# Kernel optimization log

Measured on AMD Instinct MI355X. Metric: run time of the kernel, lower is better.

The kernel has to match this reference:

```python
import jax, jax.numpy as jnp
import numpy as np

T = 2048          # tokens (flattened prefill)
H = 3584          # hidden_size
NH = 16           # num query heads
NKV = 8           # num kv heads
G = NH // NKV     # GQA group size
D = 256           # head_dim
SCALE = 256.0 ** -0.5   # query_pre_attn_scalar ** -0.5
WINDOW = 1024     # sliding_window_size
CAP = 50.0        # logit softcap
BASE = 10000.0    # rope theta
NEG = -1e30


def _rope(x, positions):
    # x: [T, n, D], neox-style rotary over full head_dim
    half = D // 2
    inv_freq = 1.0 / (BASE ** (jnp.arange(0, D, 2, dtype=jnp.float32) / D))  # [half]
    ang = positions.astype(jnp.float32)[:, None] * inv_freq  # [T, half]
    cos = jnp.cos(ang)[:, None, :]  # [T,1,half]
    sin = jnp.sin(ang)[:, None, :]
    x1, x2 = x[..., :half], x[..., half:]
    return jnp.concatenate([x1 * cos - x2 * sin, x2 * cos + x1 * sin], axis=-1)


def setup_inputs() -> dict:
    key = jax.random.key(0)
    ks = jax.random.split(key, 5)
    s = 0.02
    return {
        "hidden_states": jax.random.normal(ks[0], (T, H), dtype=jnp.float32),
        "Wq": jax.random.normal(ks[1], (H, NH * D), dtype=jnp.float32) * s,
        "Wk": jax.random.normal(ks[2], (H, NKV * D), dtype=jnp.float32) * s,
        "Wv": jax.random.normal(ks[3], (H, NKV * D), dtype=jnp.float32) * s,
        "Wo": jax.random.normal(ks[4], (NH * D, H), dtype=jnp.float32) * s,
        "positions": jnp.arange(T, dtype=jnp.int32),
    }


def reference(hidden_states, Wq, Wk, Wv, Wo, positions):
    q = (hidden_states @ Wq).reshape(T, NH, D)
    k = (hidden_states @ Wk).reshape(T, NKV, D)
    v = (hidden_states @ Wv).reshape(T, NKV, D)
    q = _rope(q, positions)
    k = _rope(k, positions)

    # GQA attention: group query heads over kv heads
    qg = (q * SCALE).reshape(T, NKV, G, D)
    scores = jnp.einsum('qhgd,khd->hgqk', qg, k)  # [NKV,G,T,T]
    scores = CAP * jnp.tanh(scores / CAP)         # logit softcap

    i = jnp.arange(T)[:, None]
    j = jnp.arange(T)[None, :]
    mask = (j <= i) & (i - j < WINDOW)            # causal + sliding window
    scores = jnp.where(mask, scores, NEG)

    p = jax.nn.softmax(scores, axis=-1)
    o = jnp.einsum('hgqk,khd->qhgd', p, v).reshape(T, NH * D)
    return o @ Wo
```

## Files before the change

### kernel.cpp

```cpp
#include <hip/hip_runtime.h>
#include <math.h>

typedef __attribute__((ext_vector_type(8))) __bf16 bf16x8;
typedef __attribute__((ext_vector_type(4))) __bf16 bf16x4;
typedef __attribute__((ext_vector_type(4))) float f32x4;

#define TSEQ 2048
#define HDIM 3584
#define NQH  16
#define NKVH 8
#define DH   256
#define WIN  1024
#define QKD  (NQH * DH)
#define KVD  (NKVH * DH)
#define QKVN 8192

#define MFMA __builtin_amdgcn_mfma_f32_16x16x32_bf16

__device__ __forceinline__ void gload_lds16(const void* g, void* l) {
  __builtin_amdgcn_global_load_lds(
      (const __attribute__((address_space(1))) void*)g,
      (__attribute__((address_space(3))) void*)l, 16, 0, 0);
}


__global__ void cvt_bf16_kernel(const float* __restrict__ in,
                                __bf16* __restrict__ out, long n) {
  long i = ((long)blockIdx.x * blockDim.x + threadIdx.x) * 4;
  if (i >= n) return;
  float4 v = *reinterpret_cast<const float4*>(in + i);
  bf16x4 o4;
  o4.x = (__bf16)v.x; o4.y = (__bf16)v.y; o4.z = (__bf16)v.z; o4.w = (__bf16)v.w;
  *reinterpret_cast<bf16x4*>(out + i) = o4;
}

__global__ void transpose_all_kernel(const float* __restrict__ Wq,
                                     const float* __restrict__ Wk,
                                     const float* __restrict__ Wv,
                                     const float* __restrict__ Wo,
                                     __bf16* __restrict__ WqT,
                                     __bf16* __restrict__ WkT,
                                     __bf16* __restrict__ WvT,
                                     __bf16* __restrict__ WoT) {
  __shared__ float tile[64][65];
  int id = blockIdx.x;
  const float* src; __bf16* dst; int R, C;
  if (id < 3584)      { src = Wq; dst = WqT; R = HDIM; C = QKD; }
  else if (id < 5376) { id -= 3584; src = Wk; dst = WkT; R = HDIM; C = KVD; }
  else if (id < 7168) { id -= 5376; src = Wv; dst = WvT; R = HDIM; C = KVD; }
  else                { id -= 7168; src = Wo; dst = WoT; R = QKD; C = HDIM; }
  const int nbx = C >> 6;
  const int c0 = (id % nbx) * 64, r0 = (id / nbx) * 64;
  const int tid = threadIdx.x;
#pragma unroll
  for (int it = 0; it < 4; ++it) {
    int f = tid + it * 256;
    int row = f >> 4, c4 = (f & 15) * 4;
    float4 v = *reinterpret_cast<const float4*>(&src[(size_t)(r0 + row) * C + c0 + c4]);
    tile[row][c4] = v.x; tile[row][c4 + 1] = v.y;
    tile[row][c4 + 2] = v.z; tile[row][c4 + 3] = v.w;
  }
  __syncthreads();
#pragma unroll
  for (int it = 0; it < 2; ++it) {
    int s = tid + it * 256;
    int oc = s >> 3, rb = (s & 7) * 8;
    bf16x8 o8;
#pragma unroll
    for (int j = 0; j < 8; ++j) o8[j] = (__bf16)tile[rb + j][oc];
    *reinterpret_cast<bf16x8*>(&dst[(size_t)(c0 + oc) * R + r0 + rb]) = o8;
  }
}

__global__ void transpose_bf16_kernel(const __bf16* __restrict__ in,
                                      __bf16* __restrict__ out, int ldin, int ldout) {
  __shared__ __bf16 tile[32][33];
  const int tx = threadIdx.x, ty = threadIdx.y;
  const int c0 = blockIdx.x * 32, r0 = blockIdx.y * 32;
#pragma unroll
  for (int i = 0; i < 4; ++i)
    tile[ty + i * 8][tx] = in[(size_t)(r0 + ty + i * 8) * ldin + (c0 + tx)];
  __syncthreads();
#pragma unroll
  for (int i = 0; i < 4; ++i)
    out[(size_t)(c0 + ty + i * 8) * ldout + (r0 + tx)] = tile[tx][ty + i * 8];
}

__global__ void rope_table_kernel(const int* __restrict__ positions,
                                  float* __restrict__ ct,
                                  float* __restrict__ st) {
  int i = blockIdx.x * blockDim.x + threadIdx.x;
  if (i >= TSEQ * 128) return;
  int t = i >> 7, j = i & 127;
  float invf = (float)exp((double)(-2 * j) * (9.210340371976184 / 256.0));
  float ang = (float)positions[t] * invf;
  ct[i] = cosf(ang);
  st[i] = sinf(ang);
}

__global__ void rope_qk_kernel(__bf16* __restrict__ qkv,
                               const float* __restrict__ ct,
                               const float* __restrict__ st) {
  int i = blockIdx.x * blockDim.x + threadIdx.x;
  int j = i & 127;
  int th = i >> 7;
  int t = th / 24;
  int hh = th - t * 24;
  float scale = (hh < 16) ? 0.0625f : 1.0f;
  size_t base = (size_t)t * QKVN + ((hh < 16) ? hh * DH : QKD + (hh - 16) * DH) + j;
  float x1 = (float)qkv[base], x2 = (float)qkv[base + 128];
  float c = ct[(t << 7) + j], s = st[(t << 7) + j];
  qkv[base]       = (__bf16)((x1 * c - x2 * s) * scale);
  qkv[base + 128] = (__bf16)((x2 * c + x1 * s) * scale);
}

__global__ void reduce2_kernel(const __bf16* __restrict__ p0,
                               const __bf16* __restrict__ p1,
                               float* __restrict__ out, int n8) {
  int stride = gridDim.x * blockDim.x;
  for (int i = blockIdx.x * blockDim.x + threadIdx.x; i < n8; i += stride) {
    bf16x8 a = reinterpret_cast<const bf16x8*>(p0)[i];
    bf16x8 b = reinterpret_cast<const bf16x8*>(p1)[i];
    float4 o0, o1;
    o0.x = (float)a[0] + (float)b[0]; o0.y = (float)a[1] + (float)b[1];
    o0.z = (float)a[2] + (float)b[2]; o0.w = (float)a[3] + (float)b[3];
    o1.x = (float)a[4] + (float)b[4]; o1.y = (float)a[5] + (float)b[5];
    o1.z = (float)a[6] + (float)b[6]; o1.w = (float)a[7] + (float)b[7];
    reinterpret_cast<float4*>(out)[2 * i] = o0;
    reinterpret_cast<float4*>(out)[2 * i + 1] = o1;
  }
}


__device__ __forceinline__ void stage_half(const __bf16* __restrict__ gbase,
                                           int row0, int ldg, int k0,
                                           __bf16* lds_half, int tid) {
  const int lane = tid & 63;
  const int w = tid >> 6;
  const int lr = lane >> 3;
  const int swzcol = ((lane & 7) ^ lr) << 3;
  const __bf16* g = gbase + (size_t)(row0 + w * 8 + lr) * ldg + k0 + swzcol;
  __bf16* l = lds_half + w * 512;
  gload_lds16(g, l);
  gload_lds16(g + (size_t)64 * ldg, l + 4096);
}

#define BAR __builtin_amdgcn_s_barrier()

#define RD_A(DST, BASE, MO)                                         \
  _Pragma("unroll")                                                 \
  for (int m_ = 0; m_ < 4; ++m_) {                                  \
    const __bf16* p_ = (BASE) + (((MO) + m_) * 16 + l15) * 64;      \
    DST[m_][0] = *(const bf16x8*)(p_ + kxa);                        \
    DST[m_][1] = *(const bf16x8*)(p_ + kxb);                        \
  }

#define RD_B(DST, BASE, NO)                                         \
  _Pragma("unroll")                                                 \
  for (int n_ = 0; n_ < 2; ++n_) {                                  \
    const __bf16* p_ = (BASE) + (bro + ((NO) + n_) * 16 + l15) * 64;\
    DST[n_][0] = *(const bf16x8*)(p_ + kxa);                        \
    DST[n_][1] = *(const bf16x8*)(p_ + kxb);                        \
  }

#define MQUAD(AF, BF, MO, NO)                                          \
  __builtin_amdgcn_s_setprio(1);                                       \
  _Pragma("unroll")                                                    \
  for (int m_ = 0; m_ < 4; ++m_)                                       \
    _Pragma("unroll")                                                  \
    for (int n_ = 0; n_ < 2; ++n_) {                                   \
      acc[(MO) + m_][(NO) + n_] =                                      \
          MFMA(AF[m_][0], BF[n_][0], acc[(MO) + m_][(NO) + n_], 0, 0, 0); \
      acc[(MO) + m_][(NO) + n_] =                                      \
          MFMA(AF[m_][1], BF[n_][1], acc[(MO) + m_][(NO) + n_], 0, 0, 0); \
    }                                                                  \
  __builtin_amdgcn_s_setprio(0);

template <typename CT>
__global__ __launch_bounds__(512, 2) void gemm256_kernel(
    const __bf16* __restrict__ A, const __bf16* __restrict__ B,
    CT* __restrict__ C, int lda, int Klen, int ldc, int nrc, size_t cstride) {
  __shared__ __bf16 lds[2][2][2][8192];

  const int nwg = gridDim.x;
  const int per = nwg >> 3;
  const int wg = (blockIdx.x & 7) * per + (blockIdx.x >> 3);
  const int kslice = wg / nrc;
  const int rem = wg - kslice * nrc;
  const int row0 = (rem & 7) * 256;
  const int col0 = (rem >> 3) * 256;
  const int k0 = kslice * Klen;
  CT* Cs = C + (size_t)kslice * cstride;

  const int tid = threadIdx.x;
  const int lane = tid & 63, w = tid >> 6;
  const int wr = w >> 2, wc = w & 3;
  const int l15 = lane & 15, lg = lane >> 4;
  const int swz = (lane & 7) << 3;
  const int kxa = (lg * 8) ^ swz;
  const int kxb = (32 + lg * 8) ^ swz;
  const int bro = (wc & 1) * 64;

  const __bf16* Ablk = A + (size_t)row0 * lda + k0;
  const __bf16* Bblk = B + (size_t)col0 * lda + k0;

  const __bf16* Ae = &lds[0][0][wr][0];
  const __bf16* Be = &lds[0][1][wc >> 1][0];
  const __bf16* Ao = &lds[1][0][wr][0];
  const __bf16* Bo = &lds[1][1][wc >> 1][0];

  f32x4 acc[8][4] = {};
  const int NT = Klen >> 6;
  const int NI = NT >> 1;

  stage_half(Ablk, 0,   lda, 0,  &lds[0][0][0][0], tid);
  stage_half(Ablk, 128, lda, 0,  &lds[0][0][1][0], tid);
  stage_half(Bblk, 0,   lda, 0,  &lds[0][1][0][0], tid);
  stage_half(Bblk, 128, lda, 0,  &lds[0][1][1][0], tid);
  stage_half(Ablk, 0,   lda, 64, &lds[1][0][0][0], tid);
  stage_half(Ablk, 128, lda, 64, &lds[1][0][1][0], tid);
  asm volatile("s_waitcnt vmcnt(4)" ::: "memory");
  BAR;

  bf16x8 a03[4][2], a47[4][2], b01[2][2], b23[2][2];

  for (int j = 0; j < NI; ++j) {
    const int e = 2 * j, o = 2 * j + 1;
    const bool last = (j == NI - 1);

    RD_A(a03, Ae, 0);
    RD_B(b01, Be, 0);
    stage_half(Bblk, 0, lda, o * 64, &lds[1][1][0][0], tid);
    asm volatile("s_waitcnt lgkmcnt(8)" ::: "memory");
    BAR; MQUAD(a03, b01, 0, 0); BAR;

    RD_A(a47, Ae, 4);
    stage_half(Bblk, 128, lda, o * 64, &lds[1][1][1][0], tid);
    BAR; MQUAD(a47, b01, 4, 0); BAR;

    RD_B(b23, Be, 2);
    if (!last) stage_half(Ablk, 0, lda, (e + 2) * 64, &lds[0][0][0][0], tid);
    BAR; MQUAD(a47, b23, 4, 2); BAR;

    if (!last) {
      stage_half(Ablk, 128, lda, (e + 2) * 64, &lds[0][0][1][0], tid);
      asm volatile("s_waitcnt vmcnt(4)" ::: "memory");
    } else {
      asm volatile("s_waitcnt vmcnt(0)" ::: "memory");
    }
    BAR; MQUAD(a03, b23, 0, 2); BAR;

    RD_A(a03, Ao, 0);
    RD_B(b01, Bo, 0);
    if (!last) stage_half(Bblk, 0, lda, (e + 2) * 64, &lds[0][1][0][0], tid);
    asm volatile("s_waitcnt lgkmcnt(8)" ::: "memory");
    BAR; MQUAD(a03, b01, 0, 0); BAR;

    RD_A(a47, Ao, 4);
    if (!last) stage_half(Bblk, 128, lda, (e + 2) * 64, &lds[0][1][1][0], tid);
    BAR; MQUAD(a47, b01, 4, 0); BAR;

    RD_B(b23, Bo, 2);
    if (!last) stage_half(Ablk, 0, lda, (o + 2) * 64, &lds[1][0][0][0], tid);
    BAR; MQUAD(a47, b23, 4, 2); BAR;

    if (!last) {
      stage_half(Ablk, 128, lda, (o + 2) * 64, &lds[1][0][1][0], tid);
      asm volatile("s_waitcnt vmcnt(4)" ::: "memory");
    }
    BAR; MQUAD(a03, b23, 0, 2); BAR;
  }

#pragma unroll
  for (int m = 0; m < 8; ++m)
#pragma unroll
    for (int n = 0; n < 4; ++n)
#pragma unroll
      for (int r = 0; r < 4; ++r) {
        int row = row0 + wr * 128 + m * 16 + lg * 4 + r;
        int col = col0 + wc * 64 + n * 16 + l15;
        Cs[(size_t)row * ldc + col] = (CT)acc[m][n][r];
      }
}


__device__ __forceinline__ void attn_stage(const __bf16* __restrict__ kg,
                                           const __bf16* __restrict__ vg,
                                           __bf16* Kd, __bf16* Vd, int tid) {
  const int ktr = tid >> 5;
  const int kslot = (tid & 31) ^ ktr;
  const __bf16* ks = kg + (size_t)ktr * QKVN + kslot * 8;
  __bf16* kd = Kd + tid * 8;
  const int vtr = (tid >> 3) & 7;
  const int vslot = (tid & 7) ^ vtr;
  const __bf16* vs = vg + (size_t)(tid >> 3) * TSEQ + vslot * 8;
  __bf16* vd = Vd + tid * 8;
#pragma unroll
  for (int i = 0; i < 8; ++i) {
    gload_lds16(ks + (size_t)(i * 8) * QKVN, kd + i * 2048);
    gload_lds16(vs + (size_t)(i * 32) * TSEQ, vd + i * 2048);
  }
}

__global__ __launch_bounds__(256, 1) void attn_kernel(
    const __bf16* __restrict__ q, const __bf16* __restrict__ k,
    const __bf16* __restrict__ vt, __bf16* __restrict__ o) {
  __shared__ __bf16 Klds[2][64][256];
  __shared__ __bf16 Vlds[2][256][64];
  __shared__ __bf16 Plds[4][2][16][72];

  const int tid = threadIdx.x;
  const int wave = tid >> 6;
  const int lane = tid & 63;
  const int l16 = lane & 15;
  const int lg = lane >> 4;
  const int h = blockIdx.x;
  const int qh = 2 * h + (wave >> 1);
  const int q0 = blockIdx.y << 6;
  const int qr = q0 + (wave & 1) * 32;

  const __bf16* kg0 = k + (size_t)h * DH;
  const __bf16* vg0 = vt + (size_t)(h * DH) * TSEQ;

  int t_lo = q0 - (WIN - 1);
  if (t_lo < 0) t_lo = 0;
  t_lo &= ~63;
  const int NTile = ((q0 - t_lo) >> 6) + 1;

  attn_stage(kg0 + (size_t)t_lo * QKVN, vg0 + t_lo, &Klds[0][0][0], &Vlds[0][0][0], tid);

  bf16x8 qf[2][8];
#pragma unroll
  for (int g = 0; g < 2; ++g) {
    const __bf16* qp = q + (size_t)(qr + 16 * g + l16) * QKVN + qh * DH + lg * 8;
#pragma unroll
    for (int ds = 0; ds < 8; ++ds)
      qf[g][ds] = *reinterpret_cast<const bf16x8*>(qp + ds * 32);
  }

  f32x4 accO[2][16] = {};
  float l_run[2][4] = {};

  for (int it = 0; it < NTile; ++it) {
    const int t0 = t_lo + it * 64;
    const int cur = it & 1;

    if (it + 1 < NTile) {
      attn_stage(kg0 + (size_t)(t0 + 64) * QKVN, vg0 + (t0 + 64),
                 &Klds[cur ^ 1][0][0], &Vlds[cur ^ 1][0][0], tid);
      asm volatile("s_waitcnt vmcnt(16)" ::: "memory");
    } else {
      asm volatile("s_waitcnt vmcnt(0)" ::: "memory");
    }
    __builtin_amdgcn_s_barrier();

    const __bf16* Kc = &Klds[cur][0][0];
    const __bf16* Vc = &Vlds[cur][0][0];

    f32x4 accS[2][4] = {};
#pragma unroll
    for (int ds = 0; ds < 8; ++ds)
#pragma unroll
      for (int nt = 0; nt < 4; ++nt) {
        int row = nt * 16 + l16;
        int slot = (4 * ds + lg) ^ (l16 & 7);
        bf16x8 kf = *reinterpret_cast<const bf16x8*>(Kc + row * 256 + slot * 8);
        accS[0][nt] = MFMA(qf[0][ds], kf, accS[0][nt], 0, 0, 0);
        accS[1][nt] = MFMA(qf[1][ds], kf, accS[1][nt], 0, 0, 0);
      }

#pragma unroll
    for (int g = 0; g < 2; ++g) {
      float rs[4] = {0.f, 0.f, 0.f, 0.f};
#pragma unroll
      for (int nt = 0; nt < 4; ++nt) {
        int key = t0 + nt * 16 + l16;
#pragma unroll
        for (int r = 0; r < 4; ++r) {
          int row = qr + 16 * g + lg * 4 + r;
          float t = __expf(accS[g][nt][r] * 0.04f);
          float p = __expf(-100.0f / (t + 1.0f));
          bool valid = (key <= row) && (row - key < WIN);
          p = valid ? p : 0.f;
          rs[r] += p;
          Plds[wave][g][lg * 4 + r][nt * 16 + l16] = (__bf16)p;
        }
      }
#pragma unroll
      for (int off = 1; off < 16; off <<= 1)
#pragma unroll
        for (int r = 0; r < 4; ++r)
          rs[r] += __shfl_xor(rs[r], off);
#pragma unroll
      for (int r = 0; r < 4; ++r)
        l_run[g][r] += rs[r];
    }

#pragma unroll
    for (int ks = 0; ks < 2; ++ks) {
      bf16x8 pa0 = *reinterpret_cast<const bf16x8*>(&Plds[wave][0][l16][ks * 32 + lg * 8]);
      bf16x8 pa1 = *reinterpret_cast<const bf16x8*>(&Plds[wave][1][l16][ks * 32 + lg * 8]);
#pragma unroll
      for (int nt2 = 0; nt2 < 16; ++nt2) {
        int row = nt2 * 16 + l16;
        int slot = (4 * ks + lg) ^ (l16 & 7);
        bf16x8 vb = *reinterpret_cast<const bf16x8*>(Vc + row * 64 + slot * 8);
        accO[0][nt2] = MFMA(pa0, vb, accO[0][nt2], 0, 0, 0);
        accO[1][nt2] = MFMA(pa1, vb, accO[1][nt2], 0, 0, 0);
      }
    }
    __builtin_amdgcn_s_barrier();
  }

#pragma unroll
  for (int g = 0; g < 2; ++g)
#pragma unroll
    for (int r = 0; r < 4; ++r) {
      float inv_l = 1.f / l_run[g][r];
      int row = qr + 16 * g + lg * 4 + r;
#pragma unroll
      for (int nt2 = 0; nt2 < 16; ++nt2)
        o[(size_t)row * QKD + qh * DH + nt2 * 16 + l16] = (__bf16)(accO[g][nt2][r] * inv_l);
    }
}


extern "C" void kernel_launch(void* const* d_in, const int* in_sizes, int n_in,
                              void* d_out, int out_size, void* d_ws, size_t ws_size,
                              hipStream_t stream) {
  const float* hs = (const float*)d_in[0];
  const float* Wq = (const float*)d_in[1];
  const float* Wk = (const float*)d_in[2];
  const float* Wv = (const float*)d_in[3];
  const float* Wo = (const float*)d_in[4];
  const int* positions = (const int*)d_in[5];
  float* out = (float*)d_out;

  char* ws = (char*)d_ws;
  const size_t SZ_HS  = (size_t)TSEQ * HDIM * 2;
  const size_t SZ_WQT = (size_t)QKD * HDIM * 2;
  const size_t SZ_WKT = (size_t)KVD * HDIM * 2;
  const size_t SZ_WOT = (size_t)HDIM * QKD * 2;
  const size_t SZ_QKV = (size_t)TSEQ * QKVN * 2;
  const size_t SZ_O   = (size_t)TSEQ * QKD * 2;
  const size_t SZ_TBL = (size_t)TSEQ * 128 * 4;

  __bf16* hs_bf = (__bf16*)ws; ws += SZ_HS;
  __bf16* WqT   = (__bf16*)ws; ws += SZ_WQT;
  __bf16* WkT   = (__bf16*)ws; ws += SZ_WKT;
  __bf16* WvT   = (__bf16*)ws; ws += SZ_WKT;
  __bf16* WoT   = (__bf16*)ws; ws += SZ_WOT;
  __bf16* qkv   = (__bf16*)ws; ws += SZ_QKV;
  __bf16* o_bf  = (__bf16*)ws; ws += SZ_O;
  float*  cost  = (float*)ws;  ws += SZ_TBL;
  float*  sint  = (float*)ws;  ws += SZ_TBL;
  __bf16* vt_bf = hs_bf;
  __bf16* cpart = WqT;
  if ((size_t)(ws - (char*)d_ws) > ws_size) return;

  cvt_bf16_kernel<<<(TSEQ * HDIM) / 1024, 256, 0, stream>>>(hs, hs_bf, (long)TSEQ * HDIM);
  transpose_all_kernel<<<10752, 256, 0, stream>>>(Wq, Wk, Wv, Wo, WqT, WkT, WvT, WoT);
  rope_table_kernel<<<(TSEQ * 128) / 256, 256, 0, stream>>>(positions, cost, sint);

  gemm256_kernel<__bf16><<<256, 512, 0, stream>>>(hs_bf, WqT, qkv, HDIM, HDIM, QKVN, 256, 0);

  rope_qk_kernel<<<(TSEQ * 24 * 128) / 256, 256, 0, stream>>>(qkv, cost, sint);
  transpose_bf16_kernel<<<dim3(KVD / 32, TSEQ / 32), dim3(32, 8), 0, stream>>>(qkv + QKD + KVD, vt_bf, QKVN, TSEQ);

  attn_kernel<<<dim3(NKVH, TSEQ / 64), 256, 0, stream>>>(qkv, qkv + QKD, vt_bf, o_bf);

  gemm256_kernel<__bf16><<<224, 512, 0, stream>>>(o_bf, WoT, cpart, QKD, QKD / 2, HDIM, 112,
                                                  (size_t)TSEQ * HDIM);
  reduce2_kernel<<<2048, 256, 0, stream>>>(cpart, cpart + (size_t)TSEQ * HDIM, out,
                                           TSEQ * HDIM / 8);
}
```

Measured before the change: 340.4 us.

## Double attention waves per block and vectorize RoPE kernel

The attention kernel now runs 8 waves per block, each owning 16 query rows instead of 32. This halves per-wave accumulator registers and adds more waves to hide latency, and the K/V staging is split across 512 threads. MFMA phases are wrapped in s_setprio raises. The RoPE kernel now processes 8 elements per thread with 128-bit loads and stores. The cost is that each K/V fragment in LDS is read by twice as many waves, raising LDS traffic per MFMA.

```diff
diff --git a/kernel.cpp b/kernel.cpp
--- a/kernel.cpp
+++ b/kernel.cpp
@@ -102,16 +102,26 @@
                                const float* __restrict__ ct,
                                const float* __restrict__ st) {
   int i = blockIdx.x * blockDim.x + threadIdx.x;
-  int j = i & 127;
-  int th = i >> 7;
+  int jg = (i & 15) * 8;
+  int th = i >> 4;
   int t = th / 24;
   int hh = th - t * 24;
   float scale = (hh < 16) ? 0.0625f : 1.0f;
-  size_t base = (size_t)t * QKVN + ((hh < 16) ? hh * DH : QKD + (hh - 16) * DH) + j;
-  float x1 = (float)qkv[base], x2 = (float)qkv[base + 128];
-  float c = ct[(t << 7) + j], s = st[(t << 7) + j];
-  qkv[base]       = (__bf16)((x1 * c - x2 * s) * scale);
-  qkv[base + 128] = (__bf16)((x2 * c + x1 * s) * scale);
+  size_t base = (size_t)t * QKVN + ((hh < 16) ? hh * DH : QKD + (hh - 16) * DH) + jg;
+  bf16x8 x1 = *reinterpret_cast<const bf16x8*>(qkv + base);
+  bf16x8 x2 = *reinterpret_cast<const bf16x8*>(qkv + base + 128);
+  const float* cp = ct + (t << 7) + jg;
+  const float* sp = st + (t << 7) + jg;
+  bf16x8 o1, o2;
+#pragma unroll
+  for (int e = 0; e < 8; ++e) {
+    float c = cp[e], s = sp[e];
+    float a = (float)x1[e], b = (float)x2[e];
+    o1[e] = (__bf16)((a * c - b * s) * scale);
+    o2[e] = (__bf16)((b * c + a * s) * scale);
+  }
+  *reinterpret_cast<bf16x8*>(qkv + base) = o1;
+  *reinterpret_cast<bf16x8*>(qkv + base + 128) = o2;
 }
 
 __global__ void reduce2_kernel(const __bf16* __restrict__ p0,
@@ -287,27 +297,22 @@
 __device__ __forceinline__ void attn_stage(const __bf16* __restrict__ kg,
                                            const __bf16* __restrict__ vg,
                                            __bf16* Kd, __bf16* Vd, int tid) {
-  const int ktr = tid >> 5;
-  const int kslot = (tid & 31) ^ ktr;
-  const __bf16* ks = kg + (size_t)ktr * QKVN + kslot * 8;
-  __bf16* kd = Kd + tid * 8;
-  const int vtr = (tid >> 3) & 7;
-  const int vslot = (tid & 7) ^ vtr;
-  const __bf16* vs = vg + (size_t)(tid >> 3) * TSEQ + vslot * 8;
-  __bf16* vd = Vd + tid * 8;
-#pragma unroll
-  for (int i = 0; i < 8; ++i) {
-    gload_lds16(ks + (size_t)(i * 8) * QKVN, kd + i * 2048);
-    gload_lds16(vs + (size_t)(i * 32) * TSEQ, vd + i * 2048);
-  }
-}
-
-__global__ __launch_bounds__(256, 1) void attn_kernel(
+#pragma unroll
+  for (int i = 0; i < 4; ++i) {
+    int c = tid + i * 512;
+    int krow = c >> 5, kslot = c & 31;
+    gload_lds16(kg + (size_t)krow * QKVN + ((kslot ^ (krow & 7)) * 8), Kd + c * 8);
+    int vrow = c >> 3, vslot = c & 7;
+    gload_lds16(vg + (size_t)vrow * TSEQ + ((vslot ^ (vrow & 7)) * 8), Vd + c * 8);
+  }
+}
+
+__global__ __launch_bounds__(512, 1) void attn_kernel(
     const __bf16* __restrict__ q, const __bf16* __restrict__ k,
     const __bf16* __restrict__ vt, __bf16* __restrict__ o) {
   __shared__ __bf16 Klds[2][64][256];
   __shared__ __bf16 Vlds[2][256][64];
-  __shared__ __bf16 Plds[4][2][16][72];
+  __shared__ __bf16 Plds[8][16][72];
 
   const int tid = threadIdx.x;
   const int wave = tid >> 6;
@@ -315,9 +320,9 @@
   const int l16 = lane & 15;
   const int lg = lane >> 4;
   const int h = blockIdx.x;
-  const int qh = 2 * h + (wave >> 1);
+  const int qh = 2 * h + (wave >> 2);
   const int q0 = blockIdx.y << 6;
-  const int qr = q0 + (wave & 1) * 32;
+  const int qr = q0 + (wave & 3) * 16;
 
   const __bf16* kg0 = k + (size_t)h * DH;
   const __bf16* vg0 = vt + (size_t)(h * DH) * TSEQ;
@@ -329,17 +334,16 @@
 
   attn_stage(kg0 + (size_t)t_lo * QKVN, vg0 + t_lo, &Klds[0][0][0], &Vlds[0][0][0], tid);
 
-  bf16x8 qf[2][8];
-#pragma unroll
-  for (int g = 0; g < 2; ++g) {
-    const __bf16* qp = q + (size_t)(qr + 16 * g + l16) * QKVN + qh * DH + lg * 8;
+  bf16x8 qf[8];
+  {
+    const __bf16* qp = q + (size_t)(qr + l16) * QKVN + qh * DH + lg * 8;
 #pragma unroll
     for (int ds = 0; ds < 8; ++ds)
-      qf[g][ds] = *reinterpret_cast<const bf16x8*>(qp + ds * 32);
-  }
-
-  f32x4 accO[2][16] = {};
-  float l_run[2][4] = {};
+      qf[ds] = *reinterpret_cast<const bf16x8*>(qp + ds * 32);
+  }
+
+  f32x4 accO[16] = {};
+  float l_run[4] = {0.f, 0.f, 0.f, 0.f};
 
   for (int it = 0; it < NTile; ++it) {
     const int t0 = t_lo + it * 64;
@@ -348,7 +352,7 @@
     if (it + 1 < NTile) {
       attn_stage(kg0 + (size_t)(t0 + 64) * QKVN, vg0 + (t0 + 64),
                  &Klds[cur ^ 1][0][0], &Vlds[cur ^ 1][0][0], tid);
-      asm volatile("s_waitcnt vmcnt(16)" ::: "memory");
+      asm volatile("s_waitcnt vmcnt(8)" ::: "memory");
     } else {
       asm volatile("s_waitcnt vmcnt(0)" ::: "memory");
     }
@@ -357,7 +361,8 @@
     const __bf16* Kc = &Klds[cur][0][0];
     const __bf16* Vc = &Vlds[cur][0][0];
 
-    f32x4 accS[2][4] = {};
+    f32x4 accS[4] = {};
+    __builtin_amdgcn_s_setprio(1);
 #pragma unroll
     for (int ds = 0; ds < 8; ++ds)
 #pragma unroll
@@ -365,63 +370,58 @@
         int row = nt * 16 + l16;
         int slot = (4 * ds + lg) ^ (l16 & 7);
         bf16x8 kf = *reinterpret_cast<const bf16x8*>(Kc + row * 256 + slot * 8);
-        accS[0][nt] = MFMA(qf[0][ds], kf, accS[0][nt], 0, 0, 0);
-        accS[1][nt] = MFMA(qf[1][ds], kf, accS[1][nt], 0, 0, 0);
+        accS[nt] = MFMA(qf[ds], kf, accS[nt], 0, 0, 0);
       }
-
-#pragma unroll
-    for (int g = 0; g < 2; ++g) {
-      float rs[4] = {0.f, 0.f, 0.f, 0.f};
-#pragma unroll
-      for (int nt = 0; nt < 4; ++nt) {
-        int key = t0 + nt * 16 + l16;
-#pragma unroll
-        for (int r = 0; r < 4; ++r) {
-          int row = qr + 16 * g + lg * 4 + r;
-          float t = __expf(accS[g][nt][r] * 0.04f);
-          float p = __expf(-100.0f / (t + 1.0f));
-          bool valid = (key <= row) && (row - key < WIN);
-          p = valid ? p : 0.f;
-          rs[r] += p;
-          Plds[wave][g][lg * 4 + r][nt * 16 + l16] = (__bf16)p;
-        }
+    __builtin_amdgcn_s_setprio(0);
+
+    float rs[4] = {0.f, 0.f, 0.f, 0.f};
+#pragma unroll
+    for (int nt = 0; nt < 4; ++nt) {
+      int key = t0 + nt * 16 + l16;
+#pragma unroll
+      for (int r = 0; r < 4; ++r) {
+        int row = qr + lg * 4 + r;
+        float t = __expf(accS[nt][r] * 0.04f);
+        float p = __expf(-100.0f / (t + 1.0f));
+        bool valid = (key <= row) && (row - key < WIN);
+        p = valid ? p : 0.f;
+        rs[r] += p;
+        Plds[wave][lg * 4 + r][nt * 16 + l16] = (__bf16)p;
       }
-#pragma unroll
-      for (int off = 1; off < 16; off <<= 1)
-#pragma unroll
-        for (int r = 0; r < 4; ++r)
-          rs[r] += __shfl_xor(rs[r], off);
+    }
+#pragma unroll
+    for (int off = 1; off < 16; off <<= 1)
 #pragma unroll
       for (int r = 0; r < 4; ++r)
-        l_run[g][r] += rs[r];
-    }
-
+        rs[r] += __shfl_xor(rs[r], off);
+#pragma unroll
+    for (int r = 0; r < 4; ++r)
+      l_run[r] += rs[r];
+
+    __builtin_amdgcn_s_setprio(1);
 #pragma unroll
     for (int ks = 0; ks < 2; ++ks) {
-      bf16x8 pa0 = *reinterpret_cast<const bf16x8*>(&Plds[wave][0][l16][ks * 32 + lg * 8]);
-      bf16x8 pa1 = *reinterpret_cast<const bf16x8*>(&Plds[wave][1][l16][ks * 32 + lg * 8]);
+      bf16x8 pa = *reinterpret_cast<const bf16x8*>(&Plds[wave][l16][ks * 32 + lg * 8]);
 #pragma unroll
       for (int nt2 = 0; nt2 < 16; ++nt2) {
         int row = nt2 * 16 + l16;
         int slot = (4 * ks + lg) ^ (l16 & 7);
         bf16x8 vb = *reinterpret_cast<const bf16x8*>(Vc + row * 64 + slot * 8);
-        accO[0][nt2] = MFMA(pa0, vb, accO[0][nt2], 0, 0, 0);
-        accO[1][nt2] = MFMA(pa1, vb, accO[1][nt2], 0, 0, 0);
+        accO[nt2] = MFMA(pa, vb, accO[nt2], 0, 0, 0);
       }
     }
+    __builtin_amdgcn_s_setprio(0);
     __builtin_amdgcn_s_barrier();
   }
 
 #pragma unroll
-  for (int g = 0; g < 2; ++g)
-#pragma unroll
-    for (int r = 0; r < 4; ++r) {
-      float inv_l = 1.f / l_run[g][r];
-      int row = qr + 16 * g + lg * 4 + r;
-#pragma unroll
-      for (int nt2 = 0; nt2 < 16; ++nt2)
-        o[(size_t)row * QKD + qh * DH + nt2 * 16 + l16] = (__bf16)(accO[g][nt2][r] * inv_l);
-    }
+  for (int r = 0; r < 4; ++r) {
+    float inv_l = 1.f / l_run[r];
+    int row = qr + lg * 4 + r;
+#pragma unroll
+    for (int nt2 = 0; nt2 < 16; ++nt2)
+      o[(size_t)row * QKD + qh * DH + nt2 * 16 + l16] = (__bf16)(accO[nt2][r] * inv_l);
+  }
 }
 
 
@@ -464,10 +464,10 @@
 
   gemm256_kernel<__bf16><<<256, 512, 0, stream>>>(hs_bf, WqT, qkv, HDIM, HDIM, QKVN, 256, 0);
 
-  rope_qk_kernel<<<(TSEQ * 24 * 128) / 256, 256, 0, stream>>>(qkv, cost, sint);
+  rope_qk_kernel<<<(TSEQ * 24 * 16) / 256, 256, 0, stream>>>(qkv, cost, sint);
   transpose_bf16_kernel<<<dim3(KVD / 32, TSEQ / 32), dim3(32, 8), 0, stream>>>(qkv + QKD + KVD, vt_bf, QKVN, TSEQ);
 
-  attn_kernel<<<dim3(NKVH, TSEQ / 64), 256, 0, stream>>>(qkv, qkv + QKD, vt_bf, o_bf);
+  attn_kernel<<<dim3(NKVH, TSEQ / 64), 512, 0, stream>>>(qkv, qkv + QKD, vt_bf, o_bf);
 
   gemm256_kernel<__bf16><<<224, 512, 0, stream>>>(o_bf, WoT, cpart, QKD, QKD / 2, HDIM, 112,
                                                   (size_t)TSEQ * HDIM);
```

New measurement: 309.5 us. 9.1% less time.
